# Optimization experiments

Hardware: AMD Instinct MI355X
Metric: run time of the kernel (lower is better)

## Reference

```python
import jax, jax.numpy as jnp
import numpy as np

EPS = 1e-8  # matches F.cosine_similarity eps clamp

def _cosine_gram(x):
    # row-normalize with eps clamp, then Gram matrix == pairwise cosine similarity
    norms = jnp.maximum(jnp.linalg.norm(x, axis=-1, keepdims=True), EPS)
    xn = x / norms
    return xn @ xn.T  # [N, N]

def setup_inputs() -> dict:
    key = jax.random.key(0)
    k1, k2 = jax.random.split(key)
    N, D = 4096, 512
    return {
        "cosine_distance_latent": jax.random.normal(k1, (N, D), dtype=jnp.float32),
        "mse_latent": jax.random.normal(k2, (N, D), dtype=jnp.float32),
    }

def reference(cosine_distance_latent, mse_latent):
    # cosine distance matrices: (sim - 1) * -1 == 1 - sim
    cd = 1.0 - _cosine_gram(cosine_distance_latent)  # target
    ed = 1.0 - _cosine_gram(mse_latent)              # predicted
    # KL(softmax(cd) || softmax(ed)) per row, then mean
    log_t = jax.nn.log_softmax(cd, axis=-1)
    log_p = jax.nn.log_softmax(ed, axis=-1)
    t = jnp.exp(log_t)
    kl = jnp.sum(t * (log_t - log_p), axis=-1)
    return jnp.mean(kl)
```

## Files before the change

### kernel.cpp

```cpp
#include <hip/hip_runtime.h>
#include <math.h>

#define NROWS 4096
#define DIM   512
#define UNIT_I 128
#define UNIT_J 64
#define NPI   (NROWS / UNIT_I)
#define NGRAINS 1056
#define KSTEPS (DIM / 32)
#define NSLOT 64

typedef __bf16 bf16x8 __attribute__((ext_vector_type(8)));
typedef float  f32x4  __attribute__((ext_vector_type(4)));

#define GL16(G, L) __builtin_amdgcn_global_load_lds( \
    (const __attribute__((address_space(1))) void*)(G), \
    (__attribute__((address_space(3))) void*)(L), 16, 0, 0)

__global__ __launch_bounds__(256)
void normalize_kernel(const float* __restrict__ X, const float* __restrict__ Y,
                      __bf16* __restrict__ Xn, __bf16* __restrict__ Yn)
{
    const int wid  = threadIdx.x >> 6;
    const int lane = threadIdx.x & 63;
    const int row  = blockIdx.x * 4 + wid;
    const float* src = blockIdx.y ? Y : X;
    __bf16*      dst = blockIdx.y ? Yn : Xn;

    const float4* s4 = reinterpret_cast<const float4*>(src + (size_t)row * DIM);
    float4 v0 = s4[lane * 2 + 0];
    float4 v1 = s4[lane * 2 + 1];
    float ss = v0.x*v0.x + v0.y*v0.y + v0.z*v0.z + v0.w*v0.w
             + v1.x*v1.x + v1.y*v1.y + v1.z*v1.z + v1.w*v1.w;
    #pragma unroll
    for (int m = 1; m < 64; m <<= 1) ss += __shfl_xor(ss, m);
    const float scale = 1.0f / fmaxf(sqrtf(ss), 1e-8f);

    bf16x8 o;
    o[0] = (__bf16)(v0.x * scale); o[1] = (__bf16)(v0.y * scale);
    o[2] = (__bf16)(v0.z * scale); o[3] = (__bf16)(v0.w * scale);
    o[4] = (__bf16)(v1.x * scale); o[5] = (__bf16)(v1.y * scale);
    o[6] = (__bf16)(v1.z * scale); o[7] = (__bf16)(v1.w * scale);
    *reinterpret_cast<bf16x8*>(dst + (size_t)row * DIM + lane * 8) = o;
}

__global__ __launch_bounds__(256, 3)
void gram_kl_kernel(const __bf16* __restrict__ Xn, const __bf16* __restrict__ Yn,
                    float4* __restrict__ partials)
{
    __shared__ char lds[49152];

    const int tid  = threadIdx.x;
    const int wid  = tid >> 6;
    const int lane = tid & 63;
    const int m  = wid >> 1;
    const int iq = wid & 1;

    const int gl = (blockIdx.x & 7) * (NGRAINS / 8) + (blockIdx.x >> 3);
    int p = (int)((sqrtf((float)(4 * gl + 1)) - 1.0f) * 0.5f);
    while ((p + 1) * (p + 2) <= gl) ++p;
    while (p * (p + 1) > gl) --p;
    const int q = gl - p * (p + 1);
    const int i0 = p * UNIT_I;
    const int j0 = q * UNIT_J;
    const int diag = (p == (q >> 1));

    const int xnib = (((tid & 3) ^ ((tid >> 3) & 3)) << 4);
    const int r0 = tid >> 2;
    const size_t so_i = ((size_t)(i0 + r0) << 10) + xnib;
    const size_t so_j = ((size_t)(j0 + r0) << 10) + xnib;
    const int wbase = wid * 1024;

    const char* bx = (const char*)Xn;
    const char* by = (const char*)Yn;

    auto STAGE = [&](int st, int ks) {
        char* base = &lds[st * 24576];
        const size_t ko = (size_t)ks << 6;
        const size_t h = (size_t)64 << 10;
        GL16(bx + so_j + ko,     base + 0     + wbase);
        GL16(by + so_j + ko,     base + 4096  + wbase);
        GL16(bx + so_i + ko,     base + 8192  + wbase);
        GL16(bx + so_i + h + ko, base + 12288 + wbase);
        GL16(by + so_i + ko,     base + 16384 + wbase);
        GL16(by + so_i + h + ko, base + 20480 + wbase);
    };

    const int rdx = ((lane & 15) << 6) + ((((lane >> 4) ^ ((lane >> 1) & 3))) << 4);

    f32x4 acc[4][4];
    #pragma unroll
    for (int fj = 0; fj < 4; ++fj)
        #pragma unroll
        for (int fi = 0; fi < 4; ++fi)
            acc[fj][fi] = f32x4{0.f, 0.f, 0.f, 0.f};

    STAGE(0, 0);

    for (int s = 0; s < KSTEPS; ++s) {
        asm volatile("s_waitcnt vmcnt(0)" ::: "memory");
        __builtin_amdgcn_s_barrier();
        asm volatile("" ::: "memory");

        const char* base = &lds[(s & 1) * 24576];
        const char* jb = base + m * 4096;
        const char* ib = base + 8192 + m * 8192 + iq * 4096;

        bf16x8 aJ[4], bI[4];
        #pragma unroll
        for (int fj = 0; fj < 4; ++fj)
            aJ[fj] = *reinterpret_cast<const bf16x8*>(jb + fj * 1024 + rdx);
        #pragma unroll
        for (int fi = 0; fi < 4; ++fi)
            bI[fi] = *reinterpret_cast<const bf16x8*>(ib + fi * 1024 + rdx);

        if (s + 1 < KSTEPS) STAGE((s + 1) & 1, s + 1);

        #pragma unroll
        for (int fj = 0; fj < 4; ++fj)
            #pragma unroll
            for (int fi = 0; fi < 4; ++fi)
                acc[fj][fi] = __builtin_amdgcn_mfma_f32_16x16x32_bf16(aJ[fj], bI[fi], acc[fj][fi], 0, 0, 0);
    }

    char*  chunk = &lds[0];
    float* jpart = reinterpret_cast<float*>(&lds[8192]);

    const int sub = lane >> 4;
    float Si[4] = {0,0,0,0}, Ui[4] = {0,0,0,0}, Vi[4] = {0,0,0,0}, Qi[4] = {0,0,0,0};

    __syncthreads();

    #pragma unroll
    for (int fj = 0; fj < 4; ++fj) {
        if (m == 1) {
            #pragma unroll
            for (int fi = 0; fi < 4; ++fi)
                *reinterpret_cast<f32x4*>(chunk + iq * 4096 + fi * 1024 + lane * 16) = acc[fj][fi];
        }
        __syncthreads();
        if (m == 0) {
            float js[4][4];
            #pragma unroll
            for (int r = 0; r < 4; ++r) { js[r][0]=0; js[r][1]=0; js[r][2]=0; js[r][3]=0; }
            #pragma unroll
            for (int fi = 0; fi < 4; ++fi) {
                const f32x4 pb = *reinterpret_cast<const f32x4*>(chunk + iq * 4096 + fi * 1024 + lane * 16);
                #pragma unroll
                for (int r = 0; r < 4; ++r) {
                    const float a = -acc[fj][fi][r];
                    const float b = -pb[r];
                    const float ea = __expf(a);
                    const float eb = __expf(b);
                    Si[fi] += ea; Ui[fi] += ea * a; Vi[fi] += ea * b; Qi[fi] += eb;
                    js[r][0] += ea; js[r][1] += ea * a; js[r][2] += ea * b; js[r][3] += eb;
                }
            }
            if (!diag) {
                #pragma unroll
                for (int r = 0; r < 4; ++r)
                    #pragma unroll
                    for (int c = 0; c < 4; ++c) {
                        #pragma unroll
                        for (int mk = 1; mk <= 8; mk <<= 1)
                            js[r][c] += __shfl_xor(js[r][c], mk);
                    }
                if ((lane & 15) == 0) {
                    #pragma unroll
                    for (int r = 0; r < 4; ++r) {
                        const int j = fj * 16 + sub * 4 + r;
                        #pragma unroll
                        for (int c = 0; c < 4; ++c)
                            jpart[(iq * 64 + j) * 4 + c] = js[r][c];
                    }
                }
            }
        }
        __syncthreads();
    }

    if (m == 0) {
        #pragma unroll
        for (int fi = 0; fi < 4; ++fi) {
            #pragma unroll
            for (int mk = 16; mk <= 32; mk <<= 1) {
                Si[fi] += __shfl_xor(Si[fi], mk);
                Ui[fi] += __shfl_xor(Ui[fi], mk);
                Vi[fi] += __shfl_xor(Vi[fi], mk);
                Qi[fi] += __shfl_xor(Qi[fi], mk);
            }
        }
        if (lane < 16) {
            #pragma unroll
            for (int fi = 0; fi < 4; ++fi) {
                const int row = i0 + iq * 64 + fi * 16 + lane;
                partials[(size_t)row * NSLOT + q] = float4{Si[fi], Ui[fi], Vi[fi], Qi[fi]};
            }
        }
    }
    __syncthreads();

    if (!diag && wid == 0) {
        const int j = lane;
        const int mslot = (q >> 1) + p + 1;
        float4 v;
        v.x = jpart[(0 * 64 + j) * 4 + 0] + jpart[(1 * 64 + j) * 4 + 0];
        v.y = jpart[(0 * 64 + j) * 4 + 1] + jpart[(1 * 64 + j) * 4 + 1];
        v.z = jpart[(0 * 64 + j) * 4 + 2] + jpart[(1 * 64 + j) * 4 + 2];
        v.w = jpart[(0 * 64 + j) * 4 + 3] + jpart[(1 * 64 + j) * 4 + 3];
        partials[(size_t)(j0 + j) * NSLOT + mslot] = v;
    }
}

__global__ __launch_bounds__(256)
void merge_kernel(const float4* __restrict__ partials, float* __restrict__ blocksum)
{
    __shared__ float w[4];
    const int row = blockIdx.x * 256 + threadIdx.x;
    const int nsl = (row >> 7) + 33;
    float S = 0.f, U = 0.f, V = 0.f, Q = 0.f;
    for (int s = 0; s < nsl; ++s) {
        const float4 pp = partials[(size_t)row * NSLOT + s];
        S += pp.x; U += pp.y; V += pp.z; Q += pp.w;
    }
    float kl = (U - V) / S - logf(S) + logf(Q);
    #pragma unroll
    for (int mm = 1; mm < 64; mm <<= 1) kl += __shfl_xor(kl, mm);
    if ((threadIdx.x & 63) == 0) w[threadIdx.x >> 6] = kl;
    __syncthreads();
    if (threadIdx.x == 0) blocksum[blockIdx.x] = w[0] + w[1] + w[2] + w[3];
}

__global__ __launch_bounds__(64)
void reduce_kernel(const float* __restrict__ blocksum, float* __restrict__ out)
{
    float v = (threadIdx.x < 16) ? blocksum[threadIdx.x] : 0.f;
    #pragma unroll
    for (int mm = 1; mm < 16; mm <<= 1) v += __shfl_xor(v, mm);
    if (threadIdx.x == 0) out[0] = v / (float)NROWS;
}

extern "C" void kernel_launch(void* const* d_in, const int* in_sizes, int n_in,
                              void* d_out, int out_size, void* d_ws, size_t ws_size,
                              hipStream_t stream)
{
    const float* X = (const float*)d_in[0];
    const float* Y = (const float*)d_in[1];
    float* out = (float*)d_out;

    char* ws = (char*)d_ws;
    const size_t mat_bytes = (size_t)NROWS * DIM * sizeof(__bf16);
    __bf16* Xn = (__bf16*)ws;
    __bf16* Yn = (__bf16*)(ws + mat_bytes);
    float4* partials = (float4*)(ws + 2 * mat_bytes);
    float* blocksum = (float*)(ws + 2 * mat_bytes + (size_t)NROWS * NSLOT * sizeof(float4));

    normalize_kernel<<<dim3(NROWS / 4, 2), 256, 0, stream>>>(X, Y, Xn, Yn);
    gram_kl_kernel<<<NGRAINS, 256, 0, stream>>>(Xn, Yn, partials);
    merge_kernel<<<NROWS / 256, 256, 0, stream>>>(partials, blocksum);
    reduce_kernel<<<1, 64, 0, stream>>>(blocksum, out);
}
```

Before: 67.44 us.

## Give each wave private LDS staging to drop per-step block barriers

Each wave now loads its own J and I tiles into a private 16KB double-buffered LDS region instead of sharing cooperatively loaded tiles, so the per-k-step s_barrier is removed and a partial vmcnt wait keeps the next stage's loads in flight. MFMA sections are wrapped in s_setprio to favour math issue. In exchange, J tiles are loaded redundantly by the two waves that share a matrix, LDS per block grows to 64KB, and launch bounds drop from 3 to 2 blocks per CU, reducing occupancy.

```diff
diff --git a/kernel.cpp b/kernel.cpp
--- a/kernel.cpp
+++ b/kernel.cpp
@@ -5,7 +5,6 @@
 #define DIM   512
 #define UNIT_I 128
 #define UNIT_J 64
-#define NPI   (NROWS / UNIT_I)
 #define NGRAINS 1056
 #define KSTEPS (DIM / 32)
 #define NSLOT 64
@@ -44,11 +43,11 @@
     *reinterpret_cast<bf16x8*>(dst + (size_t)row * DIM + lane * 8) = o;
 }
 
-__global__ __launch_bounds__(256, 3)
+__global__ __launch_bounds__(256, 2)
 void gram_kl_kernel(const __bf16* __restrict__ Xn, const __bf16* __restrict__ Yn,
                     float4* __restrict__ partials)
 {
-    __shared__ char lds[49152];
+    __shared__ char lds[65536];
 
     const int tid  = threadIdx.x;
     const int wid  = tid >> 6;
@@ -65,25 +64,25 @@
     const int j0 = q * UNIT_J;
     const int diag = (p == (q >> 1));
 
-    const int xnib = (((tid & 3) ^ ((tid >> 3) & 3)) << 4);
-    const int r0 = tid >> 2;
-    const size_t so_i = ((size_t)(i0 + r0) << 10) + xnib;
-    const size_t so_j = ((size_t)(j0 + r0) << 10) + xnib;
-    const int wbase = wid * 1024;
+    const int xnib = (((lane & 3) ^ ((lane >> 3) & 3)) << 4);
+    const int rr = lane >> 2;
+    const size_t so_j = ((size_t)(j0 + rr) << 10) + xnib;
+    const size_t so_i = ((size_t)(i0 + iq * 64 + rr) << 10) + xnib;
 
     const char* bx = (const char*)Xn;
-    const char* by = (const char*)Yn;
+    const char* srcM = m ? (const char*)Yn : bx;
+
+    char* const wlds = &lds[wid * 16384];
 
     auto STAGE = [&](int st, int ks) {
-        char* base = &lds[st * 24576];
+        char* base = wlds + st * 8192;
         const size_t ko = (size_t)ks << 6;
-        const size_t h = (size_t)64 << 10;
-        GL16(bx + so_j + ko,     base + 0     + wbase);
-        GL16(by + so_j + ko,     base + 4096  + wbase);
-        GL16(bx + so_i + ko,     base + 8192  + wbase);
-        GL16(bx + so_i + h + ko, base + 12288 + wbase);
-        GL16(by + so_i + ko,     base + 16384 + wbase);
-        GL16(by + so_i + h + ko, base + 20480 + wbase);
+        #pragma unroll
+        for (int k2 = 0; k2 < 4; ++k2)
+            GL16(srcM + so_j + ((size_t)k2 << 14) + ko, base + k2 * 1024);
+        #pragma unroll
+        for (int k2 = 0; k2 < 4; ++k2)
+            GL16(srcM + so_i + ((size_t)k2 << 14) + ko, base + 4096 + k2 * 1024);
     };
 
     const int rdx = ((lane & 15) << 6) + ((((lane >> 4) ^ ((lane >> 1) & 3))) << 4);
@@ -98,29 +97,29 @@
     STAGE(0, 0);
 
     for (int s = 0; s < KSTEPS; ++s) {
-        asm volatile("s_waitcnt vmcnt(0)" ::: "memory");
-        __builtin_amdgcn_s_barrier();
-        asm volatile("" ::: "memory");
-
-        const char* base = &lds[(s & 1) * 24576];
-        const char* jb = base + m * 4096;
-        const char* ib = base + 8192 + m * 8192 + iq * 4096;
-
+        if (s + 1 < KSTEPS) {
+            STAGE((s + 1) & 1, s + 1);
+            asm volatile("s_waitcnt vmcnt(8)" ::: "memory");
+        } else {
+            asm volatile("s_waitcnt vmcnt(0)" ::: "memory");
+        }
+
+        const char* base = wlds + (s & 1) * 8192;
         bf16x8 aJ[4], bI[4];
         #pragma unroll
         for (int fj = 0; fj < 4; ++fj)
-            aJ[fj] = *reinterpret_cast<const bf16x8*>(jb + fj * 1024 + rdx);
+            aJ[fj] = *reinterpret_cast<const bf16x8*>(base + fj * 1024 + rdx);
         #pragma unroll
         for (int fi = 0; fi < 4; ++fi)
-            bI[fi] = *reinterpret_cast<const bf16x8*>(ib + fi * 1024 + rdx);
-
-        if (s + 1 < KSTEPS) STAGE((s + 1) & 1, s + 1);
-
+            bI[fi] = *reinterpret_cast<const bf16x8*>(base + 4096 + fi * 1024 + rdx);
+
+        __builtin_amdgcn_s_setprio(1);
         #pragma unroll
         for (int fj = 0; fj < 4; ++fj)
             #pragma unroll
             for (int fi = 0; fi < 4; ++fi)
                 acc[fj][fi] = __builtin_amdgcn_mfma_f32_16x16x32_bf16(aJ[fj], bI[fi], acc[fj][fi], 0, 0, 0);
+        __builtin_amdgcn_s_setprio(0);
     }
 
     char*  chunk = &lds[0];
```

Measured after the change: 72.27 us. +7.2%, slower.
